# Kernel optimization log

Measured on AMD Instinct MI355X. Metric: run time of the kernel, lower is better.

## Reference

```python
import jax, jax.numpy as jnp
import numpy as np
from jax import lax

STRIDE = 4

def crelu(x, b):
    # cReLU: x * (x >= bias)
    return x * (x >= b).astype(x.dtype)

def rbf_conv(x, w, stride):
    # Distance-based conv: per output pixel, dist[b,o] = sum_c ||window[b,c]-w[o,c]||_2,
    # std = std(dist over (B,O)) per pixel (torch.std, ddof=1), out = exp(-dist^2/(2 std^2)).
    B, C, H, W = x.shape
    O, Cw, kh, kw = w.shape
    Hp = (H - kh) // stride + 1
    Wp = (W - kw) // stride + 1
    # patches: [B, C*kh*kw, Hp, Wp], channel-major feature order
    patches = lax.conv_general_dilated_patches(x, (kh, kw), (stride, stride), 'VALID')
    patches = patches.reshape(B, C, kh * kw, Hp * Wp)
    wf = w.reshape(O, Cw, kh * kw)
    if Cw == 1 and C > 1:
        # RBF_Conv2d reuses the same single-channel weight for every input channel
        wf = jnp.broadcast_to(wf, (O, C, kh * kw))
    pn = (patches ** 2).sum(2)                       # [B,C,P]
    wn = (wf ** 2).sum(2)                            # [O,C]
    dot = jnp.einsum('bcfp,ocf->bocp', patches, wf)  # [B,O,C,P]
    d2 = jnp.maximum(pn[:, None] + wn[None, :, :, None] - 2.0 * dot, 1e-12)
    dist = jnp.sqrt(d2).sum(2)                       # [B,O,P] sum of per-channel L2 dists
    m = dist.mean((0, 1), keepdims=True)
    var = ((dist - m) ** 2).sum((0, 1), keepdims=True) / (B * O - 1)
    std = jnp.sqrt(var)                              # per-pixel std, ddof=1
    out = jnp.exp(-(dist ** 2) / (2.0 * std ** 2))   # gaussian RBF
    return out.reshape(B, O, Hp, Wp)

def sfm(x, shape, filt, kernel, alpha0=0.9):
    # SFM temporal filtering: weight response map by alpha^seq pattern, pool by filter, re-tile
    seg_h, seg_w = shape
    C = x.shape[1]
    rm = x.transpose(0, 2, 3, 1).reshape(-1, seg_h, seg_w, C)   # get_RM
    seq = jnp.arange(filt[0] * filt[1], dtype=x.dtype)[::-1]
    alpha = (jnp.asarray(alpha0, x.dtype) ** seq).reshape(filt)
    alpha = jnp.tile(alpha, (seg_h // filt[0], seg_w // filt[1]))[None, :, :, None]
    out = (rm * alpha).reshape(-1, seg_h // filt[0], filt[0], seg_w // filt[1], filt[1], C)
    out = out.mean(axis=(2, 4))
    return out.reshape(-1, 1, kernel[0], kernel[1])

def setup_inputs():
    key = jax.random.key(0)
    ks = jax.random.split(key, 8)
    def kaiming(k, shape):
        fan_in = int(np.prod(shape[1:]))
        bound = 1.0 / np.sqrt(fan_in)
        w = jax.random.uniform(k, shape, jnp.float32, -bound, bound)
        return w.at[0].set(0.0)  # reset_parameters zeroes filter 0
    x = jax.random.uniform(ks[0], (4096, 3, 28, 28), jnp.float32)
    rgb_w = kaiming(ks[1], (100, 3, 5, 5))
    w2 = kaiming(ks[2], (225, 1, 10, 10))
    w3 = kaiming(ks[3], (625, 1, 15, 15))
    w4 = kaiming(ks[4], (1225, 1, 25, 25))
    fcb = 1.0 / np.sqrt(1225.0)
    fc_w = jax.random.uniform(ks[5], (10, 1225), jnp.float32, -fcb, fcb)
    fc_b = jax.random.uniform(ks[6], (10,), jnp.float32, -fcb, fcb)
    return {"x": x, "rgb_w": rgb_w, "w2": w2, "w3": w3, "w4": w4, "fc_w": fc_w, "fc_b": fc_b}

def reference(x, rgb_w, w2, w3, w4, fc_w, fc_b):
    B = x.shape[0]
    out = crelu(rbf_conv(x, rgb_w, STRIDE), 0.4)   # RGB_preprocess -> [B,100,6,6]
    out = sfm(out, (6, 6), (2, 2), (10, 10))       # layer1 SFM -> [B*9,1,10,10]
    out = crelu(rbf_conv(out, w2, STRIDE), 0.1)    # -> [B*9,225,1,1]
    out = sfm(out, (3, 3), (1, 3), (15, 15))       # -> [B*3,1,15,15]
    out = crelu(rbf_conv(out, w3, STRIDE), 0.01)   # -> [B*3,625,1,1]
    out = sfm(out, (3, 1), (3, 1), (25, 25))       # -> [B,1,25,25]
    out = crelu(rbf_conv(out, w4, STRIDE), 0.01)   # -> [B,1225,1,1]
    return out.reshape(B, -1) @ fc_w.T + fc_b      # fc1 -> [B,10]
```

## Files before the change

### kernel.cpp

```cpp
#include <hip/hip_runtime.h>
#include <hip/hip_bf16.h>
#include <math.h>

#define DIV_UP(a,b) (((a)+(b)-1)/(b))
#define FSQRT(x) __builtin_amdgcn_sqrtf(x)

typedef __attribute__((ext_vector_type(8))) short short8;
typedef __attribute__((ext_vector_type(4))) float f32x4;

#define GL16(g, l) __builtin_amdgcn_global_load_lds( \
    (const __attribute__((address_space(1))) void*)(g), \
    (__attribute__((address_space(3))) void*)(l), 16, 0, 0)

__global__ __launch_bounds__(256) void w1split_kernel(
    const float* __restrict__ w, ushort* __restrict__ Wh, ushort* __restrict__ Wl,
    double* __restrict__ stats) {
    if (blockIdx.x == 0 && threadIdx.x < 78) stats[threadIdx.x] = 0.0;
    int e = blockIdx.x*256 + threadIdx.x;
    if (e >= 112*96) return;
    int o = e / 96, kk = e - o*96, c = kk >> 5, k = kk & 31;
    float v = (o < 100 && k < 25) ? w[o*75 + c*25 + k] : 0.f;
    __hip_bfloat16 hb = __float2bfloat16(v);
    float hf = __bfloat162float(hb);
    __hip_bfloat16 lb = __float2bfloat16(v - hf);
    Wh[e] = *(ushort*)&hb;
    Wl[e] = *(ushort*)&lb;
}

__global__ __launch_bounds__(64) void w1norm_kernel(
    const ushort* __restrict__ Wh, const ushort* __restrict__ Wl, float* __restrict__ wn1) {
    int j = blockIdx.x*64 + threadIdx.x;
    if (j >= 336) return;
    int o = j / 3, c = j - o*3;
    const ushort* h = Wh + o*96 + c*32;
    const ushort* l = Wl + o*96 + c*32;
    float s = 0.f;
#pragma unroll
    for (int k = 0; k < 25; ++k) {
        ushort hu = h[k], lu = l[k];
        float v = __bfloat162float(*(__hip_bfloat16*)&hu) + __bfloat162float(*(__hip_bfloat16*)&lu);
        s += v*v;
    }
    wn1[j] = s;
}

__global__ __launch_bounds__(512, 2) void rbf1_mfma(
    const float* __restrict__ x, const ushort* __restrict__ Wh, const ushort* __restrict__ Wl,
    const float* __restrict__ wn1, float* __restrict__ dist1,
    float* __restrict__ pixstat) {
    __shared__ ushort Ah[3*144*32];
    __shared__ ushort Al[3*144*32];
    __shared__ float pnl[432];
    __shared__ float rstat[8*144*2];
    int tid = threadIdx.x;
    int b4 = blockIdx.x;

    for (int i = tid; i < 8*288; i += 512) rstat[i] = 0.f;

    if (tid < 432) {
        int row = tid / 3, c = tid - row*3;
        int img = row / 36, p = row - img*36;
        int ph = p / 6, pw = p - ph*6;
        const float* xp = x + (size_t)b4*9408 + img*2352 + c*784 + (ph*28 + pw)*4;
        float arr[25];
#pragma unroll
        for (int ki = 0; ki < 5; ++ki) {
            float4 v4 = *(const float4*)(xp + ki*28);
            arr[ki*5+0] = v4.x; arr[ki*5+1] = v4.y;
            arr[ki*5+2] = v4.z; arr[ki*5+3] = v4.w;
            arr[ki*5+4] = xp[ki*28 + 4];
        }
        float pnc = 0.f;
        int tilebase = c*9216 + row*64;
        int r3 = (row >> 1) & 3;
#pragma unroll
        for (int kb = 0; kb < 4; ++kb) {
            uint4 hq, lq;
            uint* hqa = (uint*)&hq;
            uint* lqa = (uint*)&lq;
#pragma unroll
            for (int j = 0; j < 4; ++j) {
                int k0 = kb*8 + 2*j;
                float v0 = (k0 < 25) ? arr[k0] : 0.f;
                float v1 = (k0+1 < 25) ? arr[k0+1] : 0.f;
                __hip_bfloat16 h0 = __float2bfloat16(v0);
                float hf0 = __bfloat162float(h0);
                __hip_bfloat16 l0 = __float2bfloat16(v0 - hf0);
                float r0 = hf0 + __bfloat162float(l0);
                __hip_bfloat16 h1 = __float2bfloat16(v1);
                float hf1 = __bfloat162float(h1);
                __hip_bfloat16 l1 = __float2bfloat16(v1 - hf1);
                float r1 = hf1 + __bfloat162float(l1);
                pnc += r0*r0 + r1*r1;
                hqa[j] = (uint)(*(ushort*)&h0) | ((uint)(*(ushort*)&h1) << 16);
                lqa[j] = (uint)(*(ushort*)&l0) | ((uint)(*(ushort*)&l1) << 16);
            }
            int kbs = kb ^ r3;
            *(uint4*)((char*)Ah + tilebase + kbs*16) = hq;
            *(uint4*)((char*)Al + tilebase + kbs*16) = lq;
        }
        pnl[tid] = pnc;
    }
    __syncthreads();

    int lane = tid & 63, wave = tid >> 6;
    {
        int rl = lane & 15, kh = lane >> 4;
        int swz = (rl >> 1) & 3;
        int kx = (kh ^ swz) * 16;
        float* mystat = rstat + wave*288;
        int pair0 = wave*8;
        int npairs = (wave == 7) ? 7 : 8;
        int cur_nf = -1;
        short8 bh0, bh1, bh2, bl0, bl1, bl2;
        float w0 = 0.f, w1v = 0.f, w2v = 0.f;
        int o = 0; bool valid = false;
        for (int pp = 0; pp < npairs; ++pp) {
            int pair = pair0 + pp;
            int nf = pair / 9, mf = pair - nf*9;
            if (nf != cur_nf) {
                cur_nf = nf;
                o = nf*16 + rl;
                const ushort* bhp = Wh + o*96 + kh*8;
                const ushort* blp = Wl + o*96 + kh*8;
                bh0 = *(const short8*)(bhp);
                bh1 = *(const short8*)(bhp + 32);
                bh2 = *(const short8*)(bhp + 64);
                bl0 = *(const short8*)(blp);
                bl1 = *(const short8*)(blp + 32);
                bl2 = *(const short8*)(blp + 64);
                w0 = wn1[o*3]; w1v = wn1[o*3+1]; w2v = wn1[o*3+2];
                valid = (o < 100);
            }
            int rbase = (mf*16 + rl)*64;
            short8 ah0 = *(const short8*)((const char*)Ah + rbase + kx);
            short8 al0 = *(const short8*)((const char*)Al + rbase + kx);
            short8 ah1 = *(const short8*)((const char*)Ah + 9216 + rbase + kx);
            short8 al1 = *(const short8*)((const char*)Al + 9216 + rbase + kx);
            short8 ah2 = *(const short8*)((const char*)Ah + 18432 + rbase + kx);
            short8 al2 = *(const short8*)((const char*)Al + 18432 + rbase + kx);
            f32x4 a0 = {0.f,0.f,0.f,0.f}, a1 = {0.f,0.f,0.f,0.f}, a2 = {0.f,0.f,0.f,0.f};
            a0 = __builtin_amdgcn_mfma_f32_16x16x32_bf16(ah0, bh0, a0, 0, 0, 0);
            a1 = __builtin_amdgcn_mfma_f32_16x16x32_bf16(ah1, bh1, a1, 0, 0, 0);
            a2 = __builtin_amdgcn_mfma_f32_16x16x32_bf16(ah2, bh2, a2, 0, 0, 0);
            a0 = __builtin_amdgcn_mfma_f32_16x16x32_bf16(ah0, bl0, a0, 0, 0, 0);
            a1 = __builtin_amdgcn_mfma_f32_16x16x32_bf16(ah1, bl1, a1, 0, 0, 0);
            a2 = __builtin_amdgcn_mfma_f32_16x16x32_bf16(ah2, bl2, a2, 0, 0, 0);
            a0 = __builtin_amdgcn_mfma_f32_16x16x32_bf16(al0, bh0, a0, 0, 0, 0);
            a1 = __builtin_amdgcn_mfma_f32_16x16x32_bf16(al1, bh1, a1, 0, 0, 0);
            a2 = __builtin_amdgcn_mfma_f32_16x16x32_bf16(al2, bh2, a2, 0, 0, 0);
            float dsum[4], dsq[4];
            size_t base = (size_t)(b4*144 + mf*16 + kh*4)*100 + o;
#pragma unroll
            for (int r = 0; r < 4; ++r) {
                int row = mf*16 + kh*4 + r;
                float d = FSQRT(fmaxf(pnl[row*3+0] + w0  - 2.f*a0[r], 1e-12f))
                        + FSQRT(fmaxf(pnl[row*3+1] + w1v - 2.f*a1[r], 1e-12f))
                        + FSQRT(fmaxf(pnl[row*3+2] + w2v - 2.f*a2[r], 1e-12f));
                float dv = valid ? d : 0.f;
                if (valid) dist1[base + (size_t)r*100] = d;
                dsum[r] = dv; dsq[r] = dv*dv;
            }
#pragma unroll
            for (int m = 1; m <= 8; m <<= 1) {
#pragma unroll
                for (int r = 0; r < 4; ++r) {
                    dsum[r] += __shfl_xor(dsum[r], m, 64);
                    dsq[r]  += __shfl_xor(dsq[r],  m, 64);
                }
            }
            if (rl == 0) {
#pragma unroll
                for (int r = 0; r < 4; ++r) {
                    int row = mf*16 + kh*4 + r;
                    mystat[row*2]     += dsum[r];
                    mystat[row*2 + 1] += dsq[r];
                }
            }
        }
    }
    __syncthreads();
    if (tid < 72) {
        int p = tid >> 1, w = tid & 1;
        float s = 0.f;
#pragma unroll
        for (int wv = 0; wv < 8; ++wv)
#pragma unroll
            for (int g = 0; g < 4; ++g)
                s += rstat[wv*288 + (p + 36*g)*2 + w];
        pixstat[(size_t)b4*72 + 2*p + w] = s;
    }
}

__global__ __launch_bounds__(256) void finalize36_kernel(
    const float* __restrict__ pixstat, float* __restrict__ scale) {
    __shared__ double ss[256], qq[256];
    int p = blockIdx.x, tid = threadIdx.x;
    double s = 0.0, q = 0.0;
    for (int b = tid; b < 1024; b += 256) {
        s += (double)pixstat[(size_t)b*72 + 2*p];
        q += (double)pixstat[(size_t)b*72 + 2*p + 1];
    }
    ss[tid] = s; qq[tid] = q; __syncthreads();
    for (int st = 128; st > 0; st >>= 1) {
        if (tid < st) { ss[tid] += ss[tid+st]; qq[tid] += qq[tid+st]; }
        __syncthreads();
    }
    if (tid == 0) {
        const double N = 409600.0;
        double m = ss[0] / N;
        double var = (qq[0] - N*m*m) / (N - 1.0);
        scale[p] = (float)(0.5 / var);
    }
}

__global__ __launch_bounds__(256) void finalize_part_kernel(
    const double* __restrict__ part, int nb,
    float* __restrict__ scale, int scaleOff, double N) {
    __shared__ double ss[256], qq[256];
    int tid = threadIdx.x;
    double s = 0.0, q = 0.0;
    for (int i = tid; i < nb; i += 256) { s += part[2*i]; q += part[2*i+1]; }
    ss[tid] = s; qq[tid] = q; __syncthreads();
    for (int st = 128; st > 0; st >>= 1) {
        if (tid < st) { ss[tid] += ss[tid+st]; qq[tid] += qq[tid+st]; }
        __syncthreads();
    }
    if (tid == 0) {
        double m = ss[0] / N;
        double var = (qq[0] - N*m*m) / (N - 1.0);
        scale[scaleOff] = (float)(0.5 / var);
    }
}

__global__ __launch_bounds__(256) void sfm1_kernel(
    const float* __restrict__ dist1, const float* __restrict__ scale,
    float* __restrict__ y2) {
    int gid = blockIdx.x*256 + threadIdx.x;
    if (gid >= 36864*100) return;
    int c = gid % 100, n = gid / 100;
    int b = n / 9, ij = n % 9, i = ij / 3, j = ij % 3;
    const float alpha[2][2] = {{0.729f, 0.81f},{0.9f, 1.0f}};
    float acc = 0.f;
#pragma unroll
    for (int fh = 0; fh < 2; ++fh)
#pragma unroll
        for (int fw = 0; fw < 2; ++fw) {
            int p = (2*i+fh)*6 + (2*j+fw);
            float d = dist1[(size_t)b*3600 + p*100 + c];
            float v = __expf(-d*d*scale[p]);
            v = (v >= 0.4f) ? v : 0.f;
            acc += alpha[fh][fw]*v;
        }
    y2[gid] = 0.25f * acc;
}

__global__ __launch_bounds__(256) void sfm1s_kernel(
    const float* __restrict__ dist1, const float* __restrict__ scale,
    ushort* __restrict__ H, ushort* __restrict__ L, float* __restrict__ norm) {
    int wave = threadIdx.x >> 6, lane = threadIdx.x & 63;
    int n = blockIdx.x*4 + wave;
    int b = n / 9, ij = n % 9, i = ij / 3, j = ij % 3;
    const float alpha[2][2] = {{0.729f, 0.81f},{0.9f, 1.0f}};
    float s = 0.f;
#pragma unroll
    for (int q = 0; q < 2; ++q) {
        int k = lane + q*64;
        float y = 0.f;
        if (k < 100) {
            float acc = 0.f;
#pragma unroll
            for (int fh = 0; fh < 2; ++fh)
#pragma unroll
                for (int fw = 0; fw < 2; ++fw) {
                    int p = (2*i+fh)*6 + (2*j+fw);
                    float d = dist1[(size_t)b*3600 + p*100 + k];
                    float v = __expf(-d*d*scale[p]);
                    v = (v >= 0.4f) ? v : 0.f;
                    acc += alpha[fh][fw]*v;
                }
            y = 0.25f * acc;
        }
        __hip_bfloat16 hb = __float2bfloat16(y);
        float hf = __bfloat162float(hb);
        __hip_bfloat16 lb = __float2bfloat16(y - hf);
        H[(size_t)n*128 + k] = *(ushort*)&hb;
        L[(size_t)n*128 + k] = *(ushort*)&lb;
        float r = hf + __bfloat162float(lb);
        s += r*r;
    }
    for (int off = 32; off > 0; off >>= 1) s += __shfl_down(s, off, 64);
    if (lane == 0) norm[n] = s;
}

__global__ __launch_bounds__(256) void splitnorm_kernel(
    const float* __restrict__ src, ushort* __restrict__ H, ushort* __restrict__ L,
    float* __restrict__ norm, int R, int K, int Kp) {
    int wave = threadIdx.x >> 6, lane = threadIdx.x & 63;
    int row = blockIdx.x*4 + wave;
    float s = 0.f;
    if (row < R) {
        for (int k = lane; k < Kp; k += 64) {
            float v = (k < K) ? src[(size_t)row*K + k] : 0.f;
            __hip_bfloat16 hb = __float2bfloat16(v);
            float hf = __bfloat162float(hb);
            __hip_bfloat16 lb = __float2bfloat16(v - hf);
            H[(size_t)row*Kp + k] = *(ushort*)&hb;
            L[(size_t)row*Kp + k] = *(ushort*)&lb;
            float r = hf + __bfloat162float(lb);
            s += r*r;
        }
    } else {
        for (int k = lane; k < Kp; k += 64) {
            H[(size_t)row*Kp + k] = 0;
            L[(size_t)row*Kp + k] = 0;
        }
    }
    for (int off = 32; off > 0; off >>= 1) s += __shfl_down(s, off, 64);
    if (lane == 0) norm[row] = s;
}

__global__ __launch_bounds__(256) void sfm2s_kernel(
    const float* __restrict__ dist2, const float* __restrict__ scale,
    ushort* __restrict__ H, ushort* __restrict__ L, float* __restrict__ norm) {
    int wave = threadIdx.x >> 6, lane = threadIdx.x & 63;
    int n2 = blockIdx.x*4 + wave;
    int b = n2 / 3, i = n2 % 3;
    float s2 = scale[0];
    const float alphaJ[3] = {0.81f, 0.9f, 1.0f};
    float s = 0.f;
#pragma unroll
    for (int q = 0; q < 4; ++q) {
        int k = lane + q*64;
        float y = 0.f;
        if (k < 225) {
            float acc = 0.f;
#pragma unroll
            for (int j = 0; j < 3; ++j) {
                float d = dist2[((size_t)(b*9 + i*3 + j))*225 + k];
                float v = __expf(-d*d*s2);
                v = (v >= 0.1f) ? v : 0.f;
                acc += alphaJ[j]*v;
            }
            y = acc * (1.f/3.f);
        }
        __hip_bfloat16 hb = __float2bfloat16(y);
        float hf = __bfloat162float(hb);
        __hip_bfloat16 lb = __float2bfloat16(y - hf);
        H[(size_t)n2*256 + k] = *(ushort*)&hb;
        L[(size_t)n2*256 + k] = *(ushort*)&lb;
        float r = hf + __bfloat162float(lb);
        s += r*r;
    }
    for (int off = 32; off > 0; off >>= 1) s += __shfl_down(s, off, 64);
    if (lane == 0) norm[n2] = s;
}

__global__ __launch_bounds__(256) void sfm3s_kernel(
    const float* __restrict__ dist3, const float* __restrict__ scale,
    ushort* __restrict__ H, ushort* __restrict__ L, float* __restrict__ norm) {
    int wave = threadIdx.x >> 6, lane = threadIdx.x & 63;
    int b = blockIdx.x*4 + wave;
    float s3 = scale[0];
    const float alphaI[3] = {0.81f, 0.9f, 1.0f};
    float s = 0.f;
#pragma unroll
    for (int q = 0; q < 10; ++q) {
        int k = lane + q*64;
        float y = 0.f;
        if (k < 625) {
            float acc = 0.f;
#pragma unroll
            for (int i = 0; i < 3; ++i) {
                float d = dist3[((size_t)(b*3 + i))*625 + k];
                float v = __expf(-d*d*s3);
                v = (v >= 0.01f) ? v : 0.f;
                acc += alphaI[i]*v;
            }
            y = acc * (1.f/3.f);
        }
        __hip_bfloat16 hb = __float2bfloat16(y);
        float hf = __bfloat162float(hb);
        __hip_bfloat16 lb = __float2bfloat16(y - hf);
        H[(size_t)b*640 + k] = *(ushort*)&hb;
        L[(size_t)b*640 + k] = *(ushort*)&lb;
        float r = hf + __bfloat162float(lb);
        s += r*r;
    }
    for (int off = 32; off > 0; off >>= 1) s += __shfl_down(s, off, 64);
    if (lane == 0) norm[b] = s;
}

__global__ __launch_bounds__(512, 4) void distg_mfma(
    const ushort* __restrict__ Yh, const ushort* __restrict__ Yl,
    const ushort* __restrict__ Wh, const ushort* __restrict__ Wl,
    const float* __restrict__ pn, const float* __restrict__ wn,
    float* __restrict__ D, int N, int O, int Kp,
    double* __restrict__ part) {
    __shared__ ushort Ahs[4096], Als[4096], Bhs[4096], Bls[4096];
    __shared__ double wred[8][2];
    int tid = threadIdx.x, lane = tid & 63, wave = tid >> 6;
    int bn = blockIdx.x * 128, bo = blockIdx.y * 128;
    int wm = wave >> 2, wq = wave & 3;

    int rL = lane >> 2, cL = lane & 3;
    int cs = cL ^ ((rL >> 1) & 3);
    int row16 = wave*16 + rL;
    size_t aoff = (size_t)(bn + row16) * Kp + cs*8;
    size_t boff = (size_t)(bo + row16) * Kp + cs*8;
    ushort* lAh = Ahs + wave*512;
    ushort* lAl = Als + wave*512;
    ushort* lBh = Bhs + wave*512;
    ushort* lBl = Bls + wave*512;

    int rl = lane & 15, kh = lane >> 4;
    int kbs_r = kh ^ ((rl >> 1) & 3);
    int raoff[4], rboff[2];
#pragma unroll
    for (int mf = 0; mf < 4; ++mf) raoff[mf] = (wm*64 + mf*16 + rl)*64 + kbs_r*16;
#pragma unroll
    for (int nf = 0; nf < 2; ++nf) rboff[nf] = (wq*32 + nf*16 + rl)*64 + kbs_r*16;

    f32x4 acc[4][2];
#pragma unroll
    for (int mf = 0; mf < 4; ++mf)
#pragma unroll
        for (int nf = 0; nf < 2; ++nf) acc[mf][nf] = (f32x4){0.f,0.f,0.f,0.f};

    int NT = Kp >> 5;
    for (int t = 0; t < NT; ++t) {
        int k0 = t*32;
        GL16(Yh + aoff + k0, lAh);
        GL16(Yl + aoff + k0, lAl);
        GL16(Wh + boff + k0, lBh);
        GL16(Wl + boff + k0, lBl);
        __syncthreads();
        short8 a_h[4], a_l[4];
#pragma unroll
        for (int mf = 0; mf < 4; ++mf) {
            a_h[mf] = *(const short8*)((const char*)Ahs + raoff[mf]);
            a_l[mf] = *(const short8*)((const char*)Als + raoff[mf]);
        }
#pragma unroll
        for (int nf = 0; nf < 2; ++nf) {
            short8 b_h = *(const short8*)((const char*)Bhs + rboff[nf]);
            short8 b_l = *(const short8*)((const char*)Bls + rboff[nf]);
#pragma unroll
            for (int mf = 0; mf < 4; ++mf) {
                acc[mf][nf] = __builtin_amdgcn_mfma_f32_16x16x32_bf16(a_h[mf], b_h, acc[mf][nf], 0, 0, 0);
                acc[mf][nf] = __builtin_amdgcn_mfma_f32_16x16x32_bf16(a_h[mf], b_l, acc[mf][nf], 0, 0, 0);
                acc[mf][nf] = __builtin_amdgcn_mfma_f32_16x16x32_bf16(a_l[mf], b_h, acc[mf][nf], 0, 0, 0);
            }
        }
        __syncthreads();
    }

    double lsum = 0.0, lsq = 0.0;
#pragma unroll
    for (int mf = 0; mf < 4; ++mf) {
#pragma unroll
        for (int r = 0; r < 4; ++r) {
            int n = bn + wm*64 + mf*16 + kh*4 + r;
            float pv = pn[n];
#pragma unroll
            for (int nf = 0; nf < 2; ++nf) {
                int o = bo + wq*32 + nf*16 + rl;
                if (o < O) {
                    float d2 = pv + wn[o] - 2.f*acc[mf][nf][r];
                    float dd = FSQRT(fmaxf(d2, 1e-12f));
                    D[(size_t)n*O + o] = dd;
                    lsum += dd; lsq += (double)dd*dd;
                }
            }
        }
    }
    for (int off = 32; off > 0; off >>= 1) {
        lsum += __shfl_down(lsum, off, 64);
        lsq  += __shfl_down(lsq,  off, 64);
    }
    if (lane == 0) { wred[wave][0] = lsum; wred[wave][1] = lsq; }
    __syncthreads();
    if (tid == 0) {
        double s = 0.0, q = 0.0;
#pragma unroll
        for (int w = 0; w < 8; ++w) { s += wred[w][0]; q += wred[w][1]; }
        int bid = blockIdx.y * gridDim.x + blockIdx.x;
        part[2*bid]   = s;
        part[2*bid+1] = q;
    }
}

__global__ __launch_bounds__(256) void fc_kernel(
    const float* __restrict__ dist4, const float* __restrict__ scale,
    const float* __restrict__ fcw, const float* __restrict__ fcb,
    float* __restrict__ out) {
    int b = blockIdx.x;
    int tid = threadIdx.x;
    float s4 = scale[0];
    float acc[10] = {};
    for (int o = tid; o < 1225; o += 256) {
        float d = dist4[(size_t)b*1225 + o];
        float v = __expf(-d*d*s4);
        v = (v >= 0.01f) ? v : 0.f;
#pragma unroll
        for (int k = 0; k < 10; ++k) acc[k] += v * fcw[k*1225 + o];
    }
    __shared__ float red[10*256];
#pragma unroll
    for (int k = 0; k < 10; ++k) red[k*256 + tid] = acc[k];
    __syncthreads();
    for (int st = 128; st > 0; st >>= 1) {
        if (tid < st) {
#pragma unroll
            for (int k = 0; k < 10; ++k) red[k*256 + tid] += red[k*256 + tid + st];
        }
        __syncthreads();
    }
    if (tid < 10) out[b*10 + tid] = red[tid*256] + fcb[tid];
}

extern "C" void kernel_launch(void* const* d_in, const int* in_sizes, int n_in,
                              void* d_out, int out_size, void* d_ws, size_t ws_size,
                              hipStream_t stream) {
    const float* x     = (const float*)d_in[0];
    const float* rgb_w = (const float*)d_in[1];
    const float* w2    = (const float*)d_in[2];
    const float* w3    = (const float*)d_in[3];
    const float* w4    = (const float*)d_in[4];
    const float* fc_w  = (const float*)d_in[5];
    const float* fc_b  = (const float*)d_in[6];
    float* out = (float*)d_out;

    float* wsf   = (float*)d_ws;
    float* dist  = wsf;
    float* ybuf  = wsf + 14745600;
    float* pnb   = ybuf + 3686400;
    float* wnb   = pnb + 36864;
    float* scale = wnb + 1280;
    double* stats = (double*)(scale + 64);
    double* pblk  = stats + 78;
    float* wsend  = (float*)(pblk + 1152);

    ushort* W1h = (ushort*)pnb;
    ushort* W1l = W1h + 10752;
    float*  wn1 = (float*)(W1l + 10752);

    float* pixstat = ybuf;

    size_t base_floats = (size_t)(wsend - wsf);
    size_t y2_floats   = 2u * 36864u * 128u / 2u;
    bool roomy = ws_size >= (base_floats + y2_floats + 1024) * sizeof(float);

    ushort* Y2h = roomy ? (ushort*)wsend : (ushort*)(dist + 8388608);
    ushort* Y2l = Y2h + 36864*128;
    ushort* W2h = (ushort*)(dist + 8388608) + 2*36864*128;
    ushort* W2l = W2h + 256*128;
    ushort* Y3h = (ushort*)ybuf;
    ushort* Y3l = Y3h + 12288*256;
    ushort* W3h = Y3l + 12288*256;
    ushort* W3l = W3h + 640*256;
    ushort* Y4h = (ushort*)ybuf;
    ushort* Y4l = Y4h + 4096*640;
    ushort* W4h = Y4l + 4096*640;
    ushort* W4l = W4h + 1280*640;

    w1split_kernel<<<DIV_UP(112*96,256), 256, 0, stream>>>(rgb_w, W1h, W1l, stats);
    w1norm_kernel<<<DIV_UP(336,64), 64, 0, stream>>>(W1h, W1l, wn1);
    rbf1_mfma<<<1024, 512, 0, stream>>>(x, W1h, W1l, wn1, dist, pixstat);
    finalize36_kernel<<<36, 256, 0, stream>>>(pixstat, scale);

    if (roomy) {
        sfm1s_kernel<<<36864/4, 256, 0, stream>>>(dist, scale, Y2h, Y2l, pnb);
    } else {
        sfm1_kernel<<<DIV_UP(36864*100,256), 256, 0, stream>>>(dist, scale, ybuf);
        splitnorm_kernel<<<36864/4, 256, 0, stream>>>(ybuf, Y2h, Y2l, pnb, 36864, 100, 128);
    }
    splitnorm_kernel<<<256/4, 256, 0, stream>>>(w2, W2h, W2l, wnb, 225, 100, 128);

    distg_mfma<<<dim3(288,2), 512, 0, stream>>>(Y2h, Y2l, W2h, W2l, pnb, wnb, dist, 36864, 225, 128, pblk);
    finalize_part_kernel<<<1, 256, 0, stream>>>(pblk, 576, scale, 36, 8294400.0);
    sfm2s_kernel<<<12288/4, 256, 0, stream>>>(dist, scale + 36, Y3h, Y3l, pnb);

    splitnorm_kernel<<<640/4, 256, 0, stream>>>(w3, W3h, W3l, wnb, 625, 225, 256);
    distg_mfma<<<dim3(96,5), 512, 0, stream>>>(Y3h, Y3l, W3h, W3l, pnb, wnb, dist, 12288, 625, 256, pblk);
    finalize_part_kernel<<<1, 256, 0, stream>>>(pblk, 480, scale, 37, 7680000.0);
    sfm3s_kernel<<<4096/4, 256, 0, stream>>>(dist, scale + 37, Y4h, Y4l, pnb);

    splitnorm_kernel<<<1280/4, 256, 0, stream>>>(w4, W4h, W4l, wnb, 1225, 625, 640);
    distg_mfma<<<dim3(32,10), 512, 0, stream>>>(Y4h, Y4l, W4h, W4l, pnb, wnb, dist, 4096, 1225, 640, pblk);
    finalize_part_kernel<<<1, 256, 0, stream>>>(pblk, 320, scale, 38, 5017600.0);

    fc_kernel<<<4096, 256, 0, stream>>>(dist, scale + 38, fc_w, fc_b, out);
}
```

Baseline: 207.1 us.

## Split rbf1 blocks to two images each and raise occupancy

```diff
diff --git a/kernel.cpp b/kernel.cpp
--- a/kernel.cpp
+++ b/kernel.cpp
@@ -44,62 +44,72 @@
     wn1[j] = s;
 }
 
-__global__ __launch_bounds__(512, 2) void rbf1_mfma(
+__global__ __launch_bounds__(512, 4) void rbf1_mfma(
     const float* __restrict__ x, const ushort* __restrict__ Wh, const ushort* __restrict__ Wl,
     const float* __restrict__ wn1, float* __restrict__ dist1,
     float* __restrict__ pixstat) {
-    __shared__ ushort Ah[3*144*32];
-    __shared__ ushort Al[3*144*32];
-    __shared__ float pnl[432];
-    __shared__ float rstat[8*144*2];
+    __shared__ ushort Ah[3*80*32];
+    __shared__ ushort Al[3*80*32];
+    __shared__ float pnl[240];
+    __shared__ float rstat[8*72*2];
     int tid = threadIdx.x;
-    int b4 = blockIdx.x;
-
-    for (int i = tid; i < 8*288; i += 512) rstat[i] = 0.f;
-
-    if (tid < 432) {
+    int b2 = blockIdx.x;
+
+    for (int i = tid; i < 8*144; i += 512) rstat[i] = 0.f;
+
+    if (tid < 240) {
         int row = tid / 3, c = tid - row*3;
-        int img = row / 36, p = row - img*36;
-        int ph = p / 6, pw = p - ph*6;
-        const float* xp = x + (size_t)b4*9408 + img*2352 + c*784 + (ph*28 + pw)*4;
-        float arr[25];
-#pragma unroll
-        for (int ki = 0; ki < 5; ++ki) {
-            float4 v4 = *(const float4*)(xp + ki*28);
-            arr[ki*5+0] = v4.x; arr[ki*5+1] = v4.y;
-            arr[ki*5+2] = v4.z; arr[ki*5+3] = v4.w;
-            arr[ki*5+4] = xp[ki*28 + 4];
-        }
-        float pnc = 0.f;
-        int tilebase = c*9216 + row*64;
+        int tilebase = c*5120 + row*64;
         int r3 = (row >> 1) & 3;
-#pragma unroll
-        for (int kb = 0; kb < 4; ++kb) {
-            uint4 hq, lq;
-            uint* hqa = (uint*)&hq;
-            uint* lqa = (uint*)&lq;
-#pragma unroll
-            for (int j = 0; j < 4; ++j) {
-                int k0 = kb*8 + 2*j;
-                float v0 = (k0 < 25) ? arr[k0] : 0.f;
-                float v1 = (k0+1 < 25) ? arr[k0+1] : 0.f;
-                __hip_bfloat16 h0 = __float2bfloat16(v0);
-                float hf0 = __bfloat162float(h0);
-                __hip_bfloat16 l0 = __float2bfloat16(v0 - hf0);
-                float r0 = hf0 + __bfloat162float(l0);
-                __hip_bfloat16 h1 = __float2bfloat16(v1);
-                float hf1 = __bfloat162float(h1);
-                __hip_bfloat16 l1 = __float2bfloat16(v1 - hf1);
-                float r1 = hf1 + __bfloat162float(l1);
-                pnc += r0*r0 + r1*r1;
-                hqa[j] = (uint)(*(ushort*)&h0) | ((uint)(*(ushort*)&h1) << 16);
-                lqa[j] = (uint)(*(ushort*)&l0) | ((uint)(*(ushort*)&l1) << 16);
-            }
-            int kbs = kb ^ r3;
-            *(uint4*)((char*)Ah + tilebase + kbs*16) = hq;
-            *(uint4*)((char*)Al + tilebase + kbs*16) = lq;
-        }
-        pnl[tid] = pnc;
+        if (row < 72) {
+            int img = row / 36, p = row - img*36;
+            int ph = p / 6, pw = p - ph*6;
+            const float* xp = x + (size_t)b2*4704 + img*2352 + c*784 + (ph*28 + pw)*4;
+            float arr[25];
+#pragma unroll
+            for (int ki = 0; ki < 5; ++ki) {
+                float4 v4 = *(const float4*)(xp + ki*28);
+                arr[ki*5+0] = v4.x; arr[ki*5+1] = v4.y;
+                arr[ki*5+2] = v4.z; arr[ki*5+3] = v4.w;
+                arr[ki*5+4] = xp[ki*28 + 4];
+            }
+            float pnc = 0.f;
+#pragma unroll
+            for (int kb = 0; kb < 4; ++kb) {
+                uint4 hq, lq;
+                uint* hqa = (uint*)&hq;
+                uint* lqa = (uint*)&lq;
+#pragma unroll
+                for (int j = 0; j < 4; ++j) {
+                    int k0 = kb*8 + 2*j;
+                    float v0 = (k0 < 25) ? arr[k0] : 0.f;
+                    float v1 = (k0+1 < 25) ? arr[k0+1] : 0.f;
+                    __hip_bfloat16 h0 = __float2bfloat16(v0);
+                    float hf0 = __bfloat162float(h0);
+                    __hip_bfloat16 l0 = __float2bfloat16(v0 - hf0);
+                    float r0 = hf0 + __bfloat162float(l0);
+                    __hip_bfloat16 h1 = __float2bfloat16(v1);
+                    float hf1 = __bfloat162float(h1);
+                    __hip_bfloat16 l1 = __float2bfloat16(v1 - hf1);
+                    float r1 = hf1 + __bfloat162float(l1);
+                    pnc += r0*r0 + r1*r1;
+                    hqa[j] = (uint)(*(ushort*)&h0) | ((uint)(*(ushort*)&h1) << 16);
+                    lqa[j] = (uint)(*(ushort*)&l0) | ((uint)(*(ushort*)&l1) << 16);
+                }
+                int kbs = kb ^ r3;
+                *(uint4*)((char*)Ah + tilebase + kbs*16) = hq;
+                *(uint4*)((char*)Al + tilebase + kbs*16) = lq;
+            }
+            pnl[tid] = pnc;
+        } else {
+            uint4 z = {0,0,0,0};
+#pragma unroll
+            for (int kb = 0; kb < 4; ++kb) {
+                *(uint4*)((char*)Ah + tilebase + kb*16) = z;
+                *(uint4*)((char*)Al + tilebase + kb*16) = z;
+            }
+            pnl[tid] = 0.f;
+        }
     }
     __syncthreads();
 
@@ -108,16 +118,15 @@
         int rl = lane & 15, kh = lane >> 4;
         int swz = (rl >> 1) & 3;
         int kx = (kh ^ swz) * 16;
-        float* mystat = rstat + wave*288;
-        int pair0 = wave*8;
-        int npairs = (wave == 7) ? 7 : 8;
+        float* mystat = rstat + wave*144;
+        int pstart = (wave*35) >> 3;
+        int pend   = ((wave+1)*35) >> 3;
         int cur_nf = -1;
         short8 bh0, bh1, bh2, bl0, bl1, bl2;
         float w0 = 0.f, w1v = 0.f, w2v = 0.f;
         int o = 0; bool valid = false;
-        for (int pp = 0; pp < npairs; ++pp) {
-            int pair = pair0 + pp;
-            int nf = pair / 9, mf = pair - nf*9;
+        for (int p = pstart; p < pend; ++p) {
+            int nf = p / 5, mf = p - nf*5;
             if (nf != cur_nf) {
                 cur_nf = nf;
                 o = nf*16 + rl;
@@ -135,10 +144,10 @@
             int rbase = (mf*16 + rl)*64;
             short8 ah0 = *(const short8*)((const char*)Ah + rbase + kx);
             short8 al0 = *(const short8*)((const char*)Al + rbase + kx);
-            short8 ah1 = *(const short8*)((const char*)Ah + 9216 + rbase + kx);
-            short8 al1 = *(const short8*)((const char*)Al + 9216 + rbase + kx);
-            short8 ah2 = *(const short8*)((const char*)Ah + 18432 + rbase + kx);
-            short8 al2 = *(const short8*)((const char*)Al + 18432 + rbase + kx);
+            short8 ah1 = *(const short8*)((const char*)Ah + 5120 + rbase + kx);
+            short8 al1 = *(const short8*)((const char*)Al + 5120 + rbase + kx);
+            short8 ah2 = *(const short8*)((const char*)Ah + 10240 + rbase + kx);
+            short8 al2 = *(const short8*)((const char*)Al + 10240 + rbase + kx);
             f32x4 a0 = {0.f,0.f,0.f,0.f}, a1 = {0.f,0.f,0.f,0.f}, a2 = {0.f,0.f,0.f,0.f};
             a0 = __builtin_amdgcn_mfma_f32_16x16x32_bf16(ah0, bh0, a0, 0, 0, 0);
             a1 = __builtin_amdgcn_mfma_f32_16x16x32_bf16(ah1, bh1, a1, 0, 0, 0);
@@ -150,15 +159,16 @@
             a1 = __builtin_amdgcn_mfma_f32_16x16x32_bf16(al1, bh1, a1, 0, 0, 0);
             a2 = __builtin_amdgcn_mfma_f32_16x16x32_bf16(al2, bh2, a2, 0, 0, 0);
             float dsum[4], dsq[4];
-            size_t base = (size_t)(b4*144 + mf*16 + kh*4)*100 + o;
+            size_t base = (size_t)(b2*72 + mf*16 + kh*4)*100 + o;
 #pragma unroll
             for (int r = 0; r < 4; ++r) {
                 int row = mf*16 + kh*4 + r;
                 float d = FSQRT(fmaxf(pnl[row*3+0] + w0  - 2.f*a0[r], 1e-12f))
                         + FSQRT(fmaxf(pnl[row*3+1] + w1v - 2.f*a1[r], 1e-12f))
                         + FSQRT(fmaxf(pnl[row*3+2] + w2v - 2.f*a2[r], 1e-12f));
-                float dv = valid ? d : 0.f;
-                if (valid) dist1[base + (size_t)r*100] = d;
+                bool ok = valid && (row < 72);
+                float dv = ok ? d : 0.f;
+                if (ok) dist1[base + (size_t)r*100] = d;
                 dsum[r] = dv; dsq[r] = dv*dv;
             }
 #pragma unroll
@@ -173,8 +183,10 @@
 #pragma unroll
                 for (int r = 0; r < 4; ++r) {
                     int row = mf*16 + kh*4 + r;
-                    mystat[row*2]     += dsum[r];
-                    mystat[row*2 + 1] += dsq[r];
+                    if (row < 72) {
+                        mystat[row*2]     += dsum[r];
+                        mystat[row*2 + 1] += dsq[r];
+                    }
                 }
             }
         }
@@ -184,11 +196,11 @@
         int p = tid >> 1, w = tid & 1;
         float s = 0.f;
 #pragma unroll
-        for (int wv = 0; wv < 8; ++wv)
-#pragma unroll
-            for (int g = 0; g < 4; ++g)
-                s += rstat[wv*288 + (p + 36*g)*2 + w];
-        pixstat[(size_t)b4*72 + 2*p + w] = s;
+        for (int wv = 0; wv < 8; ++wv) {
+            s += rstat[wv*144 + p*2 + w];
+            s += rstat[wv*144 + (p+36)*2 + w];
+        }
+        pixstat[(size_t)b2*72 + 2*p + w] = s;
     }
 }
 
@@ -197,7 +209,7 @@
     __shared__ double ss[256], qq[256];
     int p = blockIdx.x, tid = threadIdx.x;
     double s = 0.0, q = 0.0;
-    for (int b = tid; b < 1024; b += 256) {
+    for (int b = tid; b < 2048; b += 256) {
         s += (double)pixstat[(size_t)b*72 + 2*p];
         q += (double)pixstat[(size_t)b*72 + 2*p + 1];
     }
@@ -566,7 +578,7 @@
 
     w1split_kernel<<<DIV_UP(112*96,256), 256, 0, stream>>>(rgb_w, W1h, W1l, stats);
     w1norm_kernel<<<DIV_UP(336,64), 64, 0, stream>>>(W1h, W1l, wn1);
-    rbf1_mfma<<<1024, 512, 0, stream>>>(x, W1h, W1l, wn1, dist, pixstat);
+    rbf1_mfma<<<2048, 512, 0, stream>>>(x, W1h, W1l, wn1, dist, pixstat);
     finalize36_kernel<<<36, 256, 0, stream>>>(pixstat, scale);
 
     if (roomy) {
```

Result: slower. 214.9 us (+3.8%).
